# Kernel optimization log

Measured on AMD Instinct MI355X. Metric: run time of the kernel, lower is better.

The kernel has to match this reference:

```python
import jax, jax.numpy as jnp
import numpy as np

B, H, S, D = 4, 32, 2048, 128  # batch, heads, seq_len, d_head
D_MODEL = H * D


def setup_inputs() -> dict:
    key = jax.random.key(0)
    ks = jax.random.split(key, 6)
    return {
        "query_states": jax.random.normal(ks[0], (B, H, S, D), dtype=jnp.float32),
        "key_states": jax.random.normal(ks[1], (B, H, S, D), dtype=jnp.float32),
        "value_states": jax.random.normal(ks[2], (B, H, S, D), dtype=jnp.float32),
        "local_attn_outputs": jax.random.normal(ks[3], (B, H, S, D), dtype=jnp.float32),
        "balance_factors": jax.random.normal(ks[4], (H,), dtype=jnp.float32),
        "w_o": jax.random.normal(ks[5], (D_MODEL, D_MODEL), dtype=jnp.float32) / np.sqrt(D_MODEL),
    }


def reference(query_states, key_states, value_states, local_attn_outputs, balance_factors, w_o):
    # --- compressive memory from keys/values (elu+1 feature map) ---
    phi_k = jax.nn.elu(key_states) + 1.0                                  # [B,H,S,D]
    memory = jnp.einsum("bhsk,bhsv->bhkv", phi_k, value_states)           # [B,H,D,D]
    normalization = jnp.sum(phi_k, axis=2)                                # [B,H,D]

    # --- retrieval with query feature map, normalized ---
    phi_q = jax.nn.elu(query_states) + 1.0                                # [B,H,S,D]
    retrieved = jnp.einsum("bhsk,bhkv->bhsv", phi_q, memory)              # [B,H,S,D]
    denom = jnp.einsum("bhsk,bhk->bhs", phi_q, normalization)             # [B,H,S]
    retrieved = retrieved / denom[..., None]

    # --- sigmoid-gated combine of global (memory) and local attention ---
    gw = jax.nn.sigmoid(balance_factors)[None, :, None, None]             # global weights
    lw = jax.nn.sigmoid(1.0 - balance_factors)[None, :, None, None]      # local weights
    attn = gw * retrieved + lw * local_attn_outputs                       # [B,H,S,D]

    # [B,H,S,D] -> [B,S,H*D]
    attn = jnp.transpose(attn, (0, 2, 1, 3)).reshape(B, S, H * D)
    # o_proj: bias-free Linear, y = x @ W^T
    return attn @ w_o.T
```

## Files before the change

kernel.cpp:

```cpp
#include <hip/hip_runtime.h>
#include <hip/hip_bf16.h>

#define B_ 4
#define H_ 32
#define S_ 2048
#define D_ 128
#define DM_ 4096
#define BH_ (B_*H_)
#define M_ (B_*S_)

typedef short bf16x8 __attribute__((ext_vector_type(8)));
typedef short s16x4  __attribute__((ext_vector_type(4)));
typedef float f32x4  __attribute__((ext_vector_type(4)));

__device__ __forceinline__ float phi_f(float x) {
    return x > 0.f ? x + 1.f : __expf(x);
}

__device__ __forceinline__ short f2b(float x) {
    __hip_bfloat16 h = __float2bfloat16(x);
    return *(short*)&h;
}

__device__ __forceinline__ void gl_lds16(void* lds_uniform, const void* gptr) {
    __builtin_amdgcn_global_load_lds(
        (const __attribute__((address_space(1))) void*)gptr,
        (__attribute__((address_space(3))) void*)lds_uniform,
        16, 0, 0);
}

__global__ __launch_bounds__(256) void k1_memory(
    const float* __restrict__ Kin, const float* __restrict__ Vin,
    float* __restrict__ parts, float* __restrict__ nrm)
{
    const int split = blockIdx.x;
    const int bh = blockIdx.y;
    const int t = threadIdx.x;
    const int wave = t >> 6, lane = t & 63;
    const int lm = lane & 15, quad = lane >> 4;
    const int wm = wave >> 1, wn = wave & 1;

    __shared__ __hip_bfloat16 sVt[128*72];
    __shared__ __hip_bfloat16 sKt[128*72];

    const long base = (long)bh * S_ * D_ + (long)split * (S_/8) * D_;
    const float* Kp = Kin + base;
    const float* Vp = Vin + base;

    f32x4 acc[4][4];
#pragma unroll
    for (int i = 0; i < 4; ++i)
#pragma unroll
        for (int j = 0; j < 4; ++j) { f32x4 z = {0.f,0.f,0.f,0.f}; acc[i][j] = z; }

    float na[2][4] = {{0.f,0.f,0.f,0.f},{0.f,0.f,0.f,0.f}};

    const int si  = t & 15;
    const int dj0 = t >> 4;

    for (int c = 0; c < 4; ++c) {
        const int s0 = c*64 + si*4;
        __syncthreads();
#pragma unroll
        for (int m = 0; m < 2; ++m) {
            const int dj = dj0 + 16*m;
            const float* gK = Kp + (long)s0*D_ + dj*4;
            const float* gV = Vp + (long)s0*D_ + dj*4;
            float4 krv[4], vrv[4];
#pragma unroll
            for (int r = 0; r < 4; ++r) {
                krv[r] = *(const float4*)(gK + (long)r*D_);
                vrv[r] = *(const float4*)(gV + (long)r*D_);
            }
            const float* kf = (const float*)krv;
            const float* vf = (const float*)vrv;
#pragma unroll
            for (int cc = 0; cc < 4; ++cc) {
                float p0 = phi_f(kf[0*4+cc]), p1 = phi_f(kf[1*4+cc]);
                float p2 = phi_f(kf[2*4+cc]), p3 = phi_f(kf[3*4+cc]);
                na[m][cc] += p0 + p1 + p2 + p3;
                s16x4 pw; pw[0]=f2b(p0); pw[1]=f2b(p1); pw[2]=f2b(p2); pw[3]=f2b(p3);
                s16x4 vw; vw[0]=f2b(vf[0*4+cc]); vw[1]=f2b(vf[1*4+cc]);
                          vw[2]=f2b(vf[2*4+cc]); vw[3]=f2b(vf[3*4+cc]);
                const int d = dj*4 + cc;
                *(s16x4*)(sKt + d*72 + si*4) = pw;
                *(s16x4*)(sVt + d*72 + si*4) = vw;
            }
        }
        __syncthreads();
#pragma unroll
        for (int kh = 0; kh < 2; ++kh) {
            const int scol = kh*32 + quad*8;
            bf16x8 af[4], bfr[4];
#pragma unroll
            for (int x = 0; x < 4; ++x) {
                af[x]  = *(const bf16x8*)(sVt + (wm*64 + x*16 + lm)*72 + scol);
                bfr[x] = *(const bf16x8*)(sKt + (wn*64 + x*16 + lm)*72 + scol);
            }
#pragma unroll
            for (int mt = 0; mt < 4; ++mt)
#pragma unroll
                for (int nt = 0; nt < 4; ++nt)
                    acc[mt][nt] = __builtin_amdgcn_mfma_f32_16x16x32_bf16(
                        af[mt], bfr[nt], acc[mt][nt], 0, 0, 0);
        }
    }

#pragma unroll
    for (int m = 0; m < 2; ++m)
#pragma unroll
        for (int cc = 0; cc < 4; ++cc) {
            float v = na[m][cc];
            v += __shfl_xor(v, 1); v += __shfl_xor(v, 2);
            v += __shfl_xor(v, 4); v += __shfl_xor(v, 8);
            if (si == 0)
                atomicAdd(&nrm[bh*D_ + (dj0 + 16*m)*4 + cc], v);
        }

    float* mp = parts + ((long)split*BH_ + bh) * (D_*D_);
#pragma unroll
    for (int mt = 0; mt < 4; ++mt)
#pragma unroll
        for (int nt = 0; nt < 4; ++nt) {
            const int kcol = wn*64 + nt*16 + lm;
#pragma unroll
            for (int r = 0; r < 4; ++r) {
                const int vrow = wm*64 + mt*16 + quad*4 + r;
                mp[vrow*D_ + kcol] = acc[mt][nt][r];
            }
        }
}

__global__ __launch_bounds__(256) void k1b_finalize(
    const float* __restrict__ parts, __hip_bfloat16* __restrict__ memTb)
{
    const long g = (long)blockIdx.x*256 + threadIdx.x;
    const int bh  = (int)(g >> 11);
    const int rem = (int)(g & 2047);
    const int row = rem >> 4, seg = rem & 15;
    const int srcSeg = seg ^ (row & 15);
    const long sbase = (long)bh*(D_*D_) + row*D_ + srcSeg*8;

    f32x4 s0 = {0.f,0.f,0.f,0.f}, s1 = {0.f,0.f,0.f,0.f};
#pragma unroll
    for (int sp = 0; sp < 8; ++sp) {
        const float* p = parts + (long)sp*BH_*(D_*D_) + sbase;
        s0 += *(const f32x4*)p;
        s1 += *(const f32x4*)(p + 4);
    }
    bf16x8 ob;
#pragma unroll
    for (int j = 0; j < 4; ++j) { ob[j] = f2b(s0[j]); ob[4+j] = f2b(s1[j]); }
    *(bf16x8*)(memTb + g*8) = ob;
}

__global__ __launch_bounds__(256) void k2_retrieve(
    const float* __restrict__ Qin, const float* __restrict__ Lin,
    const float* __restrict__ bal,
    const __hip_bfloat16* __restrict__ memTb, const float* __restrict__ nrm,
    __hip_bfloat16* __restrict__ attnB)
{
    const int sc = blockIdx.x;
    const int bh = blockIdx.y;
    const int b = bh >> 5, h = bh & 31;
    const int t = threadIdx.x;
    const int wave = t >> 6, lane = t & 63;
    const int lm = lane & 15, quad = lane >> 4;
    const int wm = wave >> 1, wn = wave & 1;

    __shared__ char smem[128*132*4];
    __hip_bfloat16* sQ = (__hip_bfloat16*)smem;
    __hip_bfloat16* sM = (__hip_bfloat16*)(smem + 32768);
    float* sOut = (float*)smem;
    __shared__ float sDenP[128][8];
    __shared__ float sDen[128];

    const float* Qp = Qin + (long)bh*S_*D_ + (long)sc*128*D_;
    const float* Lp = Lin + (long)bh*S_*D_ + (long)sc*128*D_;
    const __hip_bfloat16* mb = memTb + (long)bh*(D_*D_);

#pragma unroll
    for (int i = 0; i < 8; ++i)
        gl_lds16((void*)(sM + (i*256 + wave*64)*8),
                 (const void*)(mb + (long)(i*256 + wave*64 + lane)*8));

    const int kq = t & 31;
    const float4 nq = *(const float4*)(nrm + bh*D_ + kq*4);
#pragma unroll
    for (int i = 0; i < 16; ++i) {
        const int idx = t + i*256;
        const int row = idx >> 5;
        float4 qv = *(const float4*)(Qp + (long)idx*4);
        float p0 = phi_f(qv.x), p1 = phi_f(qv.y), p2 = phi_f(qv.z), p3 = phi_f(qv.w);
        float part = p0*nq.x + p1*nq.y + p2*nq.z + p3*nq.w;
        part += __shfl_xor(part, 1);
        part += __shfl_xor(part, 2);
        if ((kq & 3) == 0) sDenP[row][kq >> 2] = part;
        const int seg = kq >> 1, half = kq & 1;
        const int off = row*128 + ((seg ^ (row & 15)) << 3) + half*4;
        s16x4 qw; qw[0]=f2b(p0); qw[1]=f2b(p1); qw[2]=f2b(p2); qw[3]=f2b(p3);
        *(s16x4*)(sQ + off) = qw;
    }
    __syncthreads();

    if (t < 128) {
        float d = 0.f;
#pragma unroll
        for (int j = 0; j < 8; ++j) d += sDenP[t][j];
        sDen[t] = d;
    }

    f32x4 acc[4][4];
#pragma unroll
    for (int i = 0; i < 4; ++i)
#pragma unroll
        for (int j = 0; j < 4; ++j) { f32x4 z = {0.f,0.f,0.f,0.f}; acc[i][j] = z; }

#pragma unroll
    for (int kh = 0; kh < 4; ++kh) {
        const int segk = kh*4 + quad;
        bf16x8 af[4], bfr[4];
#pragma unroll
        for (int x = 0; x < 4; ++x) {
            const int srow = wm*64 + x*16 + lm;
            af[x]  = *(const bf16x8*)(sQ + srow*128 + ((segk ^ (srow & 15)) << 3));
            const int vrow = wn*64 + x*16 + lm;
            bfr[x] = *(const bf16x8*)(sM + vrow*128 + ((segk ^ (vrow & 15)) << 3));
        }
#pragma unroll
        for (int mt = 0; mt < 4; ++mt)
#pragma unroll
            for (int nt = 0; nt < 4; ++nt)
                acc[mt][nt] = __builtin_amdgcn_mfma_f32_16x16x32_bf16(
                    af[mt], bfr[nt], acc[mt][nt], 0, 0, 0);
    }

    const float bv = bal[h];
    const float gw = 1.f/(1.f+__expf(-bv));
    const float lw = 1.f/(1.f+__expf(-(1.f-bv)));

    __syncthreads();
#pragma unroll
    for (int mt = 0; mt < 4; ++mt)
#pragma unroll
        for (int r = 0; r < 4; ++r) {
            const int srow = wm*64 + mt*16 + quad*4 + r;
            const float scale = gw / sDen[srow];
#pragma unroll
            for (int nt = 0; nt < 4; ++nt)
                sOut[srow*132 + wn*64 + nt*16 + lm] = acc[mt][nt][r]*scale;
        }
    __syncthreads();

    const int seg = t & 15;
#pragma unroll
    for (int i = 0; i < 8; ++i) {
        const int row = (t >> 4) + i*16;
        const float* Lr = Lp + (long)row*D_ + seg*8;
        const float* Or = sOut + row*132 + seg*8;
        float4 l0 = *(const float4*)Lr;
        float4 l1 = *(const float4*)(Lr + 4);
        f32x4 o0 = *(const f32x4*)Or;
        f32x4 o1 = *(const f32x4*)(Or + 4);
        bf16x8 ob;
        ob[0] = f2b(o0[0] + lw*l0.x); ob[1] = f2b(o0[1] + lw*l0.y);
        ob[2] = f2b(o0[2] + lw*l0.z); ob[3] = f2b(o0[3] + lw*l0.w);
        ob[4] = f2b(o1[0] + lw*l1.x); ob[5] = f2b(o1[1] + lw*l1.y);
        ob[6] = f2b(o1[2] + lw*l1.z); ob[7] = f2b(o1[3] + lw*l1.w);
        const long oidx = ((long)b*S_ + sc*128 + row)*DM_ + h*D_ + seg*8;
        *(bf16x8*)(attnB + oidx) = ob;
    }
}

__global__ __launch_bounds__(256) void kconv(
    const float* __restrict__ w, __hip_bfloat16* __restrict__ wb)
{
    long i = ((long)blockIdx.x*256 + threadIdx.x)*4;
    float4 f = *(const float4*)(w + i);
    __hip_bfloat16 ob[4] = {__float2bfloat16(f.x), __float2bfloat16(f.y),
                            __float2bfloat16(f.z), __float2bfloat16(f.w)};
    *(uint2*)(wb + i) = *(uint2*)ob;
}

#define GBM 256
#define GBN 256
#define GBK 64
#define GNT (DM_/GBK)

__device__ __forceinline__ bf16x8 ldfrag(const __hip_bfloat16* base, int row, int k) {
    const int kk = k ^ ((row & 7) << 3);
    return *(const bf16x8*)(base + row * GBK + kk);
}

__device__ __forceinline__ void stage_half(
    const __hip_bfloat16* __restrict__ G, __hip_bfloat16* sb,
    int r0g, int kb, int wave, int lane)
{
#pragma unroll
    for (int r = 0; r < 4; ++r) {
        const int c   = r * 512 + wave * 64 + lane;
        const int row = c >> 3;
        const int ko  = ((c & 7) ^ (row & 7)) * 8;
        gl_lds16((void*)(sb + (r * 512 + wave * 64) * 8),
                 (const void*)(G + (long)(r0g + row) * DM_ + kb + ko));
    }
}

__global__ __launch_bounds__(512, 2) void k3_gemm(
    const __hip_bfloat16* __restrict__ X,
    const __hip_bfloat16* __restrict__ W,
    float* __restrict__ Y)
{
    __shared__ alignas(16) __hip_bfloat16 sA[2][GBM * GBK];
    __shared__ alignas(16) __hip_bfloat16 sB[2][GBN * GBK];

    const int tid = threadIdx.x;
    const int wave = tid >> 6, lane = tid & 63;
    const int lm = lane & 15, quad = lane >> 4;
    const int wm = wave >> 2, wn = wave & 3;

    const int orig = blockIdx.x;
    const int wg = (orig & 7) * 64 + (orig >> 3);
    const int m0 = (wg >> 4) * GBM;
    const int n0 = (wg & 15) * GBN;

    f32x4 acc[8][4];
#pragma unroll
    for (int i = 0; i < 8; ++i)
#pragma unroll
        for (int j = 0; j < 4; ++j) { f32x4 z = {0.f,0.f,0.f,0.f}; acc[i][j] = z; }

    const int ar0 = wm * 128 + lm;
    const int br0 = wn * 64 + lm;
    const int kq  = quad * 8;

    stage_half(W, sB[0], n0, 0, wave, lane);
    stage_half(X, sA[0], m0, 0, wave, lane);
    stage_half(W, sB[1], n0, GBK, wave, lane);
    stage_half(X, sA[1], m0, GBK, wave, lane);
    asm volatile("s_waitcnt vmcnt(8)" ::: "memory");
    __builtin_amdgcn_s_barrier();

    bf16x8 a[4][2], b[4][2];

    for (int t = 0; t < GNT; ++t) {
        const int cur = t & 1;
        const __hip_bfloat16* As = sA[cur];
        const __hip_bfloat16* Bs = sB[cur];

#pragma unroll
        for (int mf = 0; mf < 4; ++mf)
#pragma unroll
            for (int kh = 0; kh < 2; ++kh)
                a[mf][kh] = ldfrag(As, ar0 + mf * 16, kh * 32 + kq);
#pragma unroll
        for (int nf = 0; nf < 2; ++nf)
#pragma unroll
            for (int kh = 0; kh < 2; ++kh)
                b[nf][kh] = ldfrag(Bs, br0 + nf * 16, kh * 32 + kq);
        __builtin_amdgcn_s_barrier();
        asm volatile("s_waitcnt lgkmcnt(0)" ::: "memory");
        __builtin_amdgcn_sched_barrier(0);
        __builtin_amdgcn_s_setprio(1);
#pragma unroll
        for (int mf = 0; mf < 4; ++mf)
#pragma unroll
            for (int nf = 0; nf < 2; ++nf)
#pragma unroll
                for (int kh = 0; kh < 2; ++kh)
                    acc[mf][nf] = __builtin_amdgcn_mfma_f32_16x16x32_bf16(
                        a[mf][kh], b[nf][kh], acc[mf][nf], 0, 0, 0);
        __builtin_amdgcn_s_setprio(0);
        __builtin_amdgcn_s_barrier();

#pragma unroll
        for (int nf = 2; nf < 4; ++nf)
#pragma unroll
            for (int kh = 0; kh < 2; ++kh)
                b[nf][kh] = ldfrag(Bs, br0 + nf * 16, kh * 32 + kq);
        __builtin_amdgcn_s_barrier();
        asm volatile("s_waitcnt lgkmcnt(0)" ::: "memory");
        __builtin_amdgcn_sched_barrier(0);
        __builtin_amdgcn_s_setprio(1);
#pragma unroll
        for (int mf = 0; mf < 4; ++mf)
#pragma unroll
            for (int nf = 2; nf < 4; ++nf)
#pragma unroll
                for (int kh = 0; kh < 2; ++kh)
                    acc[mf][nf] = __builtin_amdgcn_mfma_f32_16x16x32_bf16(
                        a[mf][kh], b[nf][kh], acc[mf][nf], 0, 0, 0);
        __builtin_amdgcn_s_setprio(0);
        __builtin_amdgcn_s_barrier();

        if (t + 2 < GNT)
            stage_half(W, sB[cur], n0, (t + 2) * GBK, wave, lane);
#pragma unroll
        for (int mf = 0; mf < 4; ++mf)
#pragma unroll
            for (int kh = 0; kh < 2; ++kh)
                a[mf][kh] = ldfrag(As, ar0 + 64 + mf * 16, kh * 32 + kq);
        __builtin_amdgcn_s_barrier();
        asm volatile("s_waitcnt lgkmcnt(0)" ::: "memory");
        __builtin_amdgcn_sched_barrier(0);
        __builtin_amdgcn_s_setprio(1);
#pragma unroll
        for (int mf = 0; mf < 4; ++mf)
#pragma unroll
            for (int nf = 0; nf < 2; ++nf)
#pragma unroll
                for (int kh = 0; kh < 2; ++kh)
                    acc[4 + mf][nf] = __builtin_amdgcn_mfma_f32_16x16x32_bf16(
                        a[mf][kh], b[nf][kh], acc[4 + mf][nf], 0, 0, 0);
        __builtin_amdgcn_s_setprio(0);
        __builtin_amdgcn_s_barrier();

        if (t + 2 < GNT)
            stage_half(X, sA[cur], m0, (t + 2) * GBK, wave, lane);
        __builtin_amdgcn_s_barrier();
        __builtin_amdgcn_s_setprio(1);
#pragma unroll
        for (int mf = 0; mf < 4; ++mf)
#pragma unroll
            for (int nf = 2; nf < 4; ++nf)
#pragma unroll
                for (int kh = 0; kh < 2; ++kh)
                    acc[4 + mf][nf] = __builtin_amdgcn_mfma_f32_16x16x32_bf16(
                        a[mf][kh], b[nf][kh], acc[4 + mf][nf], 0, 0, 0);
        __builtin_amdgcn_s_setprio(0);
        if (t + 2 < GNT)
            asm volatile("s_waitcnt vmcnt(8)" ::: "memory");
        else
            asm volatile("s_waitcnt vmcnt(0)" ::: "memory");
        __builtin_amdgcn_s_barrier();
    }

#pragma unroll
    for (int mf = 0; mf < 8; ++mf) {
        const int row = m0 + wm * 128 + mf * 16 + quad * 4;
#pragma unroll
        for (int nf = 0; nf < 4; ++nf) {
            const int col = n0 + wn * 64 + nf * 16 + lm;
#pragma unroll
            for (int r = 0; r < 4; ++r)
                Y[(long)(row + r) * DM_ + col] = acc[mf][nf][r];
        }
    }
}

extern "C" void kernel_launch(void* const* d_in, const int* in_sizes, int n_in,
                              void* d_out, int out_size, void* d_ws, size_t ws_size,
                              hipStream_t stream) {
    const float* Q   = (const float*)d_in[0];
    const float* K   = (const float*)d_in[1];
    const float* V   = (const float*)d_in[2];
    const float* L   = (const float*)d_in[3];
    const float* bal = (const float*)d_in[4];
    const float* Wo  = (const float*)d_in[5];
    float* Y = (float*)d_out;

    char* ws = (char*)d_ws;
    float* parts = (float*)ws;
    __hip_bfloat16* attnB = (__hip_bfloat16*)ws;
    __hip_bfloat16* woB = (__hip_bfloat16*)(ws + 67108864);
    float* nrm   = (float*)(ws + 100663296);
    __hip_bfloat16* memTb = (__hip_bfloat16*)(ws + 100728832);

    hipMemsetAsync(nrm, 0, 65536, stream);

    k1_memory<<<dim3(8, BH_), 256, 0, stream>>>(K, V, parts, nrm);
    k1b_finalize<<<1024, 256, 0, stream>>>(parts, memTb);
    kconv<<<DM_*DM_/4/256, 256, 0, stream>>>(Wo, woB);
    k2_retrieve<<<dim3(S_/128, BH_), 256, 0, stream>>>(Q, L, bal, memTb, nrm, attnB);
    k3_gemm<<<dim3(512), 512, 0, stream>>>(attnB, woB, Y);
}
```

Measured before the change: 829.1 us.

## Restructure GEMM main loop, drop memset via per-split norm partials, coarsen weight convert

The GEMM inner loop goes from four barrier-separated MFMA phases to two larger phases. Both LDS refills are issued together after a single barrier, which cuts barrier and waitcnt overhead per K-step and holds all four B fragments in registers. The norm reduction now writes per-split partials that the finalize kernel sums in extra blocks, removing the memset and the global atomics. The weight conversion kernel handles eight float4s per thread with fewer blocks. The risks are higher register pressure in the GEMM and less fine-grained overlap of LDS reads with MFMA work.

```diff
diff --git a/kernel.cpp b/kernel.cpp
--- a/kernel.cpp
+++ b/kernel.cpp
@@ -31,7 +31,7 @@
 
 __global__ __launch_bounds__(256) void k1_memory(
     const float* __restrict__ Kin, const float* __restrict__ Vin,
-    float* __restrict__ parts, float* __restrict__ nrm)
+    float* __restrict__ parts, float* __restrict__ nrmP)
 {
     const int split = blockIdx.x;
     const int bh = blockIdx.y;
@@ -113,9 +113,13 @@
             float v = na[m][cc];
             v += __shfl_xor(v, 1); v += __shfl_xor(v, 2);
             v += __shfl_xor(v, 4); v += __shfl_xor(v, 8);
-            if (si == 0)
-                atomicAdd(&nrm[bh*D_ + (dj0 + 16*m)*4 + cc], v);
-        }
+            na[m][cc] = v;
+        }
+    if (si == 0) {
+        float* np = nrmP + ((long)split*BH_ + bh)*D_;
+        *(float4*)&np[dj0*4]      = make_float4(na[0][0], na[0][1], na[0][2], na[0][3]);
+        *(float4*)&np[(dj0+16)*4] = make_float4(na[1][0], na[1][1], na[1][2], na[1][3]);
+    }
 
     float* mp = parts + ((long)split*BH_ + bh) * (D_*D_);
 #pragma unroll
@@ -132,9 +136,19 @@
 }
 
 __global__ __launch_bounds__(256) void k1b_finalize(
-    const float* __restrict__ parts, __hip_bfloat16* __restrict__ memTb)
-{
-    const long g = (long)blockIdx.x*256 + threadIdx.x;
+    const float* __restrict__ parts, const float* __restrict__ nrmP,
+    __hip_bfloat16* __restrict__ memTb, float* __restrict__ nrm)
+{
+    const int bid = blockIdx.x;
+    if (bid >= 1024) {
+        const int idx = (bid - 1024)*256 + threadIdx.x;
+        float s = 0.f;
+#pragma unroll
+        for (int sp = 0; sp < 8; ++sp) s += nrmP[(long)sp*BH_*D_ + idx];
+        nrm[idx] = s;
+        return;
+    }
+    const long g = (long)bid*256 + threadIdx.x;
     const int bh  = (int)(g >> 11);
     const int rem = (int)(g & 2047);
     const int row = rem >> 4, seg = rem & 15;
@@ -275,11 +289,15 @@
 __global__ __launch_bounds__(256) void kconv(
     const float* __restrict__ w, __hip_bfloat16* __restrict__ wb)
 {
-    long i = ((long)blockIdx.x*256 + threadIdx.x)*4;
-    float4 f = *(const float4*)(w + i);
-    __hip_bfloat16 ob[4] = {__float2bfloat16(f.x), __float2bfloat16(f.y),
-                            __float2bfloat16(f.z), __float2bfloat16(f.w)};
-    *(uint2*)(wb + i) = *(uint2*)ob;
+    const long base = (long)blockIdx.x*256 + threadIdx.x;
+#pragma unroll
+    for (int it = 0; it < 8; ++it) {
+        long i = (base + (long)it*524288)*4;
+        float4 f = *(const float4*)(w + i);
+        __hip_bfloat16 ob[4] = {__float2bfloat16(f.x), __float2bfloat16(f.y),
+                                __float2bfloat16(f.z), __float2bfloat16(f.w)};
+        *(uint2*)(wb + i) = *(uint2*)ob;
+    }
 }
 
 #define GBM 256
@@ -354,80 +372,48 @@
             for (int kh = 0; kh < 2; ++kh)
                 a[mf][kh] = ldfrag(As, ar0 + mf * 16, kh * 32 + kq);
 #pragma unroll
-        for (int nf = 0; nf < 2; ++nf)
+        for (int nf = 0; nf < 4; ++nf)
 #pragma unroll
             for (int kh = 0; kh < 2; ++kh)
                 b[nf][kh] = ldfrag(Bs, br0 + nf * 16, kh * 32 + kq);
-        __builtin_amdgcn_s_barrier();
-        asm volatile("s_waitcnt lgkmcnt(0)" ::: "memory");
-        __builtin_amdgcn_sched_barrier(0);
+
         __builtin_amdgcn_s_setprio(1);
 #pragma unroll
         for (int mf = 0; mf < 4; ++mf)
 #pragma unroll
-            for (int nf = 0; nf < 2; ++nf)
+            for (int nf = 0; nf < 4; ++nf)
 #pragma unroll
                 for (int kh = 0; kh < 2; ++kh)
                     acc[mf][nf] = __builtin_amdgcn_mfma_f32_16x16x32_bf16(
                         a[mf][kh], b[nf][kh], acc[mf][nf], 0, 0, 0);
         __builtin_amdgcn_s_setprio(0);
-        __builtin_amdgcn_s_barrier();
-
-#pragma unroll
-        for (int nf = 2; nf < 4; ++nf)
+
+#pragma unroll
+        for (int mf = 0; mf < 4; ++mf)
 #pragma unroll
             for (int kh = 0; kh < 2; ++kh)
-                b[nf][kh] = ldfrag(Bs, br0 + nf * 16, kh * 32 + kq);
-        __builtin_amdgcn_s_barrier();
+                a[mf][kh] = ldfrag(As, ar0 + 64 + mf * 16, kh * 32 + kq);
+
         asm volatile("s_waitcnt lgkmcnt(0)" ::: "memory");
         __builtin_amdgcn_sched_barrier(0);
+        __builtin_amdgcn_s_barrier();
+
+        if (t + 2 < GNT) {
+            stage_half(W, sB[cur], n0, (t + 2) * GBK, wave, lane);
+            stage_half(X, sA[cur], m0, (t + 2) * GBK, wave, lane);
+        }
+
         __builtin_amdgcn_s_setprio(1);
 #pragma unroll
         for (int mf = 0; mf < 4; ++mf)
 #pragma unroll
-            for (int nf = 2; nf < 4; ++nf)
-#pragma unroll
-                for (int kh = 0; kh < 2; ++kh)
-                    acc[mf][nf] = __builtin_amdgcn_mfma_f32_16x16x32_bf16(
-                        a[mf][kh], b[nf][kh], acc[mf][nf], 0, 0, 0);
-        __builtin_amdgcn_s_setprio(0);
-        __builtin_amdgcn_s_barrier();
-
-        if (t + 2 < GNT)
-            stage_half(W, sB[cur], n0, (t + 2) * GBK, wave, lane);
-#pragma unroll
-        for (int mf = 0; mf < 4; ++mf)
-#pragma unroll
-            for (int kh = 0; kh < 2; ++kh)
-                a[mf][kh] = ldfrag(As, ar0 + 64 + mf * 16, kh * 32 + kq);
-        __builtin_amdgcn_s_barrier();
-        asm volatile("s_waitcnt lgkmcnt(0)" ::: "memory");
-        __builtin_amdgcn_sched_barrier(0);
-        __builtin_amdgcn_s_setprio(1);
-#pragma unroll
-        for (int mf = 0; mf < 4; ++mf)
-#pragma unroll
-            for (int nf = 0; nf < 2; ++nf)
+            for (int nf = 0; nf < 4; ++nf)
 #pragma unroll
                 for (int kh = 0; kh < 2; ++kh)
                     acc[4 + mf][nf] = __builtin_amdgcn_mfma_f32_16x16x32_bf16(
                         a[mf][kh], b[nf][kh], acc[4 + mf][nf], 0, 0, 0);
         __builtin_amdgcn_s_setprio(0);
-        __builtin_amdgcn_s_barrier();
-
-        if (t + 2 < GNT)
-            stage_half(X, sA[cur], m0, (t + 2) * GBK, wave, lane);
-        __builtin_amdgcn_s_barrier();
-        __builtin_amdgcn_s_setprio(1);
-#pragma unroll
-        for (int mf = 0; mf < 4; ++mf)
-#pragma unroll
-            for (int nf = 2; nf < 4; ++nf)
-#pragma unroll
-                for (int kh = 0; kh < 2; ++kh)
-                    acc[4 + mf][nf] = __builtin_amdgcn_mfma_f32_16x16x32_bf16(
-                        a[mf][kh], b[nf][kh], acc[4 + mf][nf], 0, 0, 0);
-        __builtin_amdgcn_s_setprio(0);
+
         if (t + 2 < GNT)
             asm volatile("s_waitcnt vmcnt(8)" ::: "memory");
         else
@@ -465,12 +451,12 @@
     __hip_bfloat16* woB = (__hip_bfloat16*)(ws + 67108864);
     float* nrm   = (float*)(ws + 100663296);
     __hip_bfloat16* memTb = (__hip_bfloat16*)(ws + 100728832);
-
-    hipMemsetAsync(nrm, 0, 65536, stream);
-
-    k1_memory<<<dim3(8, BH_), 256, 0, stream>>>(K, V, parts, nrm);
-    k1b_finalize<<<1024, 256, 0, stream>>>(parts, memTb);
-    kconv<<<DM_*DM_/4/256, 256, 0, stream>>>(Wo, woB);
+    float* nrmP  = (float*)(ws + 104923136);
+
+
+    k1_memory<<<dim3(8, BH_), 256, 0, stream>>>(K, V, parts, nrmP);
+    k1b_finalize<<<1088, 256, 0, stream>>>(parts, nrmP, memTb, nrm);
+    kconv<<<2048, 256, 0, stream>>>(Wo, woB);
     k2_retrieve<<<dim3(S_/128, BH_), 256, 0, stream>>>(Q, L, bal, memTb, nrm, attnB);
     k3_gemm<<<dim3(512), 512, 0, stream>>>(attnB, woB, Y);
 }
```

Result: no change. 829.6 us (+0.1%).
